# Performance work log

Measured on AMD Instinct MI355X. Metric: run time of the kernel, lower is better.

## Reference

```python
import jax, jax.numpy as jnp
import numpy as np

BS, NMEM, NQ, D, H, NL = 16, 256, 63, 512, 512, 1
INI = 0.01

def setup_inputs() -> dict:
    key = jax.random.key(0)
    ks = jax.random.split(key, 13)
    s_ih = 1.0 / np.sqrt(H)
    return {
        "knowledge_state": jax.random.normal(ks[0], (BS, NMEM, D), jnp.float32),
        "knowledge_num": jax.random.randint(ks[1], (BS,), 1, NMEM),
        "lstm_in": jax.random.normal(ks[2], (BS, NQ, D), jnp.float32),
        "init_h": jax.random.uniform(ks[3], (NL, H), jnp.float32, -INI, INI),
        "init_c": jax.random.uniform(ks[4], (NL, H), jnp.float32, -INI, INI),
        "init_i": jax.random.uniform(ks[5], (D,), jnp.float32, -0.1, 0.1),
        "w_ih": jax.random.uniform(ks[6], (4 * H, D), jnp.float32, -s_ih, s_ih),
        "w_hh": jax.random.uniform(ks[7], (4 * H, H), jnp.float32, -s_ih, s_ih),
        "b_ih": jax.random.uniform(ks[8], (4 * H,), jnp.float32, -s_ih, s_ih),
        "b_hh": jax.random.uniform(ks[9], (4 * H,), jnp.float32, -s_ih, s_ih),
        "attn_wm": jax.random.normal(ks[10], (D, H), jnp.float32) * np.sqrt(2.0 / (D + H)),
        "attn_wq": jax.random.normal(ks[11], (H, H), jnp.float32) * np.sqrt(2.0 / (H + H)),
        "attn_v": jax.random.uniform(ks[12], (H,), jnp.float32, -INI, INI),
    }


def _lstm(x_tbd, h0, c0, w_ih, w_hh, b_ih, b_hh):
    # x_tbd: [T, bs, D]; single-layer LSTM, PyTorch gate order (i, f, g, o)
    b = b_ih + b_hh

    def step(carry, x_t):
        h, c = carry
        gates = x_t @ w_ih.T + h @ w_hh.T + b  # [bs, 4H]
        i, f, g, o = jnp.split(gates, 4, axis=-1)
        c = jax.nn.sigmoid(f) * c + jax.nn.sigmoid(i) * jnp.tanh(g)
        h = jax.nn.sigmoid(o) * jnp.tanh(c)
        return (h, c), h

    _, ys = jax.lax.scan(step, (h0, c0), x_tbd)
    return ys  # [T, bs, H]


def reference(knowledge_state, knowledge_num, lstm_in, init_h, init_c, init_i,
              w_ih, w_hh, b_ih, b_hh, attn_wm, attn_wq, attn_v):
    bs = knowledge_state.shape[0]
    # _prepare: project memory, broadcast init states
    attn_feat = jnp.einsum('bmd,dh->bmh', knowledge_state, attn_wm)  # [bs, n_mem, H]
    # prepend learned init input token, go seq-first for the LSTM
    x = jnp.concatenate(
        [jnp.broadcast_to(init_i[None, None, :], (bs, 1, init_i.shape[0])), lstm_in],
        axis=1)                                   # [bs, T, D], T = n_q + 1
    x = jnp.swapaxes(x, 0, 1)                     # [T, bs, D]
    h0 = jnp.broadcast_to(init_h[0][None, :], (bs, init_h.shape[1]))
    c0 = jnp.broadcast_to(init_c[0][None, :], (bs, init_c.shape[1]))
    ys = _lstm(x, h0, c0, w_ih, w_hh, b_ih, b_hh)  # [T, bs, H]
    query = jnp.swapaxes(ys, 0, 1)                 # [bs, T, H]
    # additive (Bahdanau) attention score
    q = jnp.einsum('bth,hk->btk', query, attn_wq)  # [bs, T, H]
    s = jnp.tanh(attn_feat[:, None, :, :] + q[:, :, None, :])  # [bs, T, n_mem, H]
    score = jnp.einsum('btmh,h->btm', s, attn_v)   # [bs, T, n_mem]
    return score
```

## Files before the change

### kernel.cpp

```cpp
#include <hip/hip_runtime.h>

#define BS   16
#define NMEM 256
#define NQ   63
#define T    64
#define D    512
#define H    512
#define G4   2048

#define K2C  2.885390081777927f

typedef __attribute__((ext_vector_type(8))) short short8;
typedef __attribute__((ext_vector_type(4))) float float4v;

enum : size_t {
    OFF_XW  = 0,
    OFF_YS  = OFF_XW  + (size_t)T*BS*G4,
    OFF_HB  = OFF_YS  + (size_t)(T+1)*BS*H,
    OFF_AF  = OFF_HB  + (size_t)(T+1)*BS*H,
    OFF_Q   = OFF_AF  + (size_t)BS*NMEM*H,
    OFF_X   = OFF_Q   + (size_t)T*BS*H,
    OFF_B   = OFF_X   + (size_t)T*BS*D,
    OFF_BAR = OFF_B   + (size_t)G4,
};

__device__ inline unsigned short bf16_rn(float x) {
    union { float f; unsigned u; } a; a.f = x;
    unsigned r = a.u + 0x7FFFu + ((a.u >> 16) & 1u);
    return (unsigned short)(r >> 16);
}
__device__ inline float bf16_to_f(unsigned short s) {
    union { float f; unsigned u; } a; a.u = ((unsigned)s) << 16;
    return a.f;
}

__global__ void prep(const float* __restrict__ lstm_in, const float* __restrict__ init_h,
                     const float* __restrict__ init_i,
                     const float* __restrict__ b_ih, const float* __restrict__ b_hh,
                     float* __restrict__ xbuf, float* __restrict__ biasbuf,
                     unsigned short* __restrict__ hb0)
{
    int i = blockIdx.x * blockDim.x + threadIdx.x;
    const int NX = T*BS*D;
    if (i < NX) {
        int d = i & 511; int r = i >> 9; int t = r >> 4; int b = r & 15;
        float v = (t == 0) ? init_i[d] : lstm_in[((size_t)(b*NQ) + (t-1))*D + d];
        __builtin_nontemporal_store(v, xbuf + i);
    } else if (i < NX + G4) {
        int j = i - NX; biasbuf[j] = b_ih[j] + b_hh[j];
    } else if (i < NX + G4 + 8192) {
        int e = i - (NX + G4);
        int iw = e & 7;
        int k = ((e >> 3) >> 4) * 8 + iw;
        float h0 = init_h[k];
        unsigned short hi = bf16_rn(h0);
        unsigned short lo = bf16_rn(h0 - bf16_to_f(hi));
        hb0[e] = hi;
        hb0[8192 + e] = lo;
    }
}

template<bool BT>
__device__ inline void gemm_unit(const float* __restrict__ A, const float* __restrict__ B,
                                 float* __restrict__ C, const float* __restrict__ bias,
                                 int N, int K, int tm, int tn, int t2)
{
    const int w = t2 >> 6, lane = t2 & 63;
    const int quad = lane >> 4, l15 = lane & 15;
    const int am = tm + w*16 + l15;
    float4v acch[4] = {{0,0,0,0},{0,0,0,0},{0,0,0,0},{0,0,0,0}};
    float4v accl[4] = {{0,0,0,0},{0,0,0,0},{0,0,0,0},{0,0,0,0}};
    for (int k0 = 0; k0 < K; k0 += 32) {
        const float* ap = A + (size_t)am*K + k0 + quad*8;
        float4 a0 = *(const float4*)ap, a1 = *(const float4*)(ap+4);
        float av[8] = {a0.x,a0.y,a0.z,a0.w,a1.x,a1.y,a1.z,a1.w};
        short8 ah, al;
#pragma unroll
        for (int i = 0; i < 8; ++i) {
            unsigned short hi = bf16_rn(av[i]);
            ah[i] = (short)hi; al[i] = (short)bf16_rn(av[i] - bf16_to_f(hi));
        }
#pragma unroll
        for (int ni = 0; ni < 4; ++ni) {
            const int n = tn + ni*16 + l15;
            float bv[8];
            if (BT) {
                const float* bp = B + (size_t)n*K + k0 + quad*8;
                float4 b0 = *(const float4*)bp, b1 = *(const float4*)(bp+4);
                bv[0]=b0.x; bv[1]=b0.y; bv[2]=b0.z; bv[3]=b0.w;
                bv[4]=b1.x; bv[5]=b1.y; bv[6]=b1.z; bv[7]=b1.w;
            } else {
                const float* bp = B + (size_t)(k0 + quad*8)*N + n;
#pragma unroll
                for (int i = 0; i < 8; ++i) bv[i] = bp[(size_t)i*N];
            }
            short8 bh, bl;
#pragma unroll
            for (int i = 0; i < 8; ++i) {
                unsigned short hi = bf16_rn(bv[i]);
                bh[i] = (short)hi; bl[i] = (short)bf16_rn(bv[i] - bf16_to_f(hi));
            }
            acch[ni] = __builtin_amdgcn_mfma_f32_16x16x32_bf16(ah, bh, acch[ni], 0, 0, 0);
            accl[ni] = __builtin_amdgcn_mfma_f32_16x16x32_bf16(al, bh, accl[ni], 0, 0, 0);
            accl[ni] = __builtin_amdgcn_mfma_f32_16x16x32_bf16(ah, bl, accl[ni], 0, 0, 0);
        }
    }
#pragma unroll
    for (int ni = 0; ni < 4; ++ni) {
        const int n = tn + ni*16 + l15;
        float bb = bias ? bias[n] : 0.f;
        float4v r = acch[ni] + accl[ni];
#pragma unroll
        for (int j = 0; j < 4; ++j) {
            int row = tm + w*16 + quad*4 + j;
            __builtin_nontemporal_store(r[j] + bb, C + (size_t)row*N + n);
        }
    }
}

template<bool BT>
__global__ __launch_bounds__(256) void gemm_mfma(const float* __restrict__ A,
                                                 const float* __restrict__ B,
                                                 float* __restrict__ C,
                                                 const float* __restrict__ bias,
                                                 int N, int K)
{
    gemm_unit<BT>(A, B, C, bias, N, K, blockIdx.y*64, blockIdx.x*64, threadIdx.x);
}

__global__ __launch_bounds__(512, 2) void lstm_af(
    const float* __restrict__ xW,
    const float* __restrict__ w_hh,
    const float* __restrict__ init_c,
    const float* __restrict__ ks,
    const float* __restrict__ wm,
    float* __restrict__ ys,
    unsigned short* __restrict__ hbuf,
    float* __restrict__ af,
    int* __restrict__ flags)
{
    const int tid = threadIdx.x;

    if (blockIdx.x >= 32) {
        const int u = tid >> 8;
        const int tau = (blockIdx.x - 32)*2 + u;
        gemm_unit<false>(ks, wm, af, nullptr, H, D, (tau >> 3)*64, (tau & 7)*64, tid & 255);
        return;
    }

    __shared__ float smem[3328];
    float* part = smem;
    float* cst  = smem + 2048;
    float* xwb  = smem + 2304;

    const int jt    = blockIdx.x;
    const int w     = tid >> 6;
    const int g     = w >> 1;
    const int khalf = w & 1;
    const int lane  = tid & 63;
    const int quad  = lane >> 4;
    const int l15   = lane & 15;

    short8 bh[8], bl[8];
    {
        const int row = g*512 + jt*16 + l15;
        const float* wr = w_hh + (size_t)row*H + khalf*256 + quad*8;
#pragma unroll
        for (int kt = 0; kt < 8; ++kt) {
            const float* wp = wr + kt*32;
#pragma unroll
            for (int i = 0; i < 8; ++i) {
                float v = wp[i];
                unsigned short hi = bf16_rn(v);
                bh[kt][i] = (short)hi;
                bl[kt][i] = (short)bf16_rn(v - bf16_to_f(hi));
            }
        }
    }

    const int b2 = tid >> 4, j16 = tid & 15;
    if (tid < 256) cst[b2*16 + j16] = init_c[jt*16 + j16];
    if (tid >= 256) {
        int ti = tid - 256;
        int bb = ti >> 4, s = ti & 15;
        int gg = s & 3, j4 = (s >> 2) << 2;
        float4 v = *(const float4*)(xW + (size_t)bb*G4 + gg*512 + jt*16 + j4);
        float* dst = xwb + gg*256 + bb*16 + j4;
        dst[0]=v.x; dst[1]=v.y; dst[2]=v.z; dst[3]=v.w;
    }
    __syncthreads();

    for (int t = 0; t < T; ++t) {
        const unsigned short* hbt = hbuf + (size_t)t*16384;
        short8 ah[8], al[8];
#pragma unroll
        for (int kt = 0; kt < 8; ++kt) {
            int c = ((khalf*8 + kt)*4 + quad)*16 + l15;
            const unsigned short* p0 = hbt + (size_t)c*8;
            const unsigned short* p1 = p0 + 8192;
            asm volatile("global_load_dwordx4 %0, %1, off sc0 sc1"
                         : "=v"(ah[kt]) : "v"(p0) : "memory");
            asm volatile("global_load_dwordx4 %0, %1, off sc0 sc1"
                         : "=v"(al[kt]) : "v"(p1) : "memory");
        }
        asm volatile("s_waitcnt vmcnt(0)" ::: "memory");
        __builtin_amdgcn_sched_barrier(0);

        float4v a0 = {0.f,0.f,0.f,0.f}, a1 = {0.f,0.f,0.f,0.f};
#pragma unroll
        for (int kt = 0; kt < 8; ++kt) {
            a0 = __builtin_amdgcn_mfma_f32_16x16x32_bf16(ah[kt], bh[kt], a0, 0, 0, 0);
            a1 = __builtin_amdgcn_mfma_f32_16x16x32_bf16(al[kt], bh[kt], a1, 0, 0, 0);
            a1 = __builtin_amdgcn_mfma_f32_16x16x32_bf16(ah[kt], bl[kt], a1, 0, 0, 0);
        }
        a0 += a1;
        *(float4v*)&part[(w*64 + lane)*4] = a0;
        __syncthreads();

        if (tid < 256) {
            const int lsrc = ((b2 >> 2)*16 + j16)*4, r = b2 & 3;
            float gi = part[(0*256) + lsrc + r] + part[(1*256) + lsrc + r] + xwb[0*256 + b2*16 + j16];
            float gf = part[(2*256) + lsrc + r] + part[(3*256) + lsrc + r] + xwb[1*256 + b2*16 + j16];
            float gg = part[(4*256) + lsrc + r] + part[(5*256) + lsrc + r] + xwb[2*256 + b2*16 + j16];
            float go = part[(6*256) + lsrc + r] + part[(7*256) + lsrc + r] + xwb[3*256 + b2*16 + j16];
            float si = 1.f/(1.f+__expf(-gi));
            float sf = 1.f/(1.f+__expf(-gf));
            float so = 1.f/(1.f+__expf(-go));
            float cn = sf*cst[b2*16 + j16] + si*tanhf(gg);
            float hn = so*tanhf(cn);
            cst[b2*16 + j16] = cn;
            __builtin_nontemporal_store(hn, ys + (size_t)(t+1)*BS*H + b2*H + jt*16 + j16);
            const int k = jt*16 + j16;
            const int e = ((k >> 3)*16 + b2)*8 + (k & 7);
            unsigned short hi = bf16_rn(hn);
            unsigned int hv = (unsigned int)hi;
            unsigned int lv = (unsigned int)bf16_rn(hn - bf16_to_f(hi));
            unsigned short* hb1 = hbuf + (size_t)(t+1)*16384;
            asm volatile("global_store_short %0, %1, off sc0 sc1"
                         :: "v"(hb1 + e), "v"(hv) : "memory");
            asm volatile("global_store_short %0, %1, off sc0 sc1"
                         :: "v"(hb1 + 8192 + e), "v"(lv) : "memory");
            asm volatile("s_waitcnt vmcnt(0)" ::: "memory");
        }
        __syncthreads();

        if (t < T-1) {
            if (tid == 0) {
                int fv = t + 1;
                asm volatile("global_store_dword %0, %1, off sc0 sc1"
                             :: "v"(flags + jt*16), "v"(fv) : "memory");
            }
            if (tid >= 256) {
                int ti = tid - 256;
                int bb = ti >> 4, s = ti & 15;
                int gg2 = s & 3, j4 = (s >> 2) << 2;
                float4 v = *(const float4*)(xW + (size_t)(t+1)*BS*G4 + bb*G4 + gg2*512 + jt*16 + j4);
                float* dst = xwb + gg2*256 + bb*16 + j4;
                dst[0]=v.x; dst[1]=v.y; dst[2]=v.z; dst[3]=v.w;
            }
            if (tid < 64) {
                const int fidx = (tid & 31) << 4;
                const int* fp = flags + fidx;
                int v;
                do {
                    asm volatile("global_load_dword %0, %1, off sc0 sc1\n\t"
                                 "s_waitcnt vmcnt(0)"
                                 : "=v"(v) : "v"(fp) : "memory");
                } while (!__all(v >= t+1));
            }
            __syncthreads();
        }
    }
}

__global__ __launch_bounds__(256) void attn(const float* __restrict__ af,
                                            const float* __restrict__ q,
                                            const float* __restrict__ v,
                                            float* __restrict__ out)
{
    __shared__ float afs[64][68];
    __shared__ float qs[4][516];
    __shared__ float vs[512];
    const int tid = threadIdx.x;
    const int mc = blockIdx.x, tc = blockIdx.y, b = blockIdx.z;
    for (int i = tid; i < 4*128; i += 256) {
        int t = i >> 7, h4 = (i & 127) << 2;
        float4 x = *(const float4*)(q + ((size_t)((tc*4 + t)*16 + b) << 9) + h4);
        x.x *= K2C; x.y *= K2C; x.z *= K2C; x.w *= K2C;
        *(float4*)&qs[t][h4] = x;
    }
    for (int i = tid; i < 128; i += 256)
        *(float4*)&vs[i << 2] = *(const float4*)(v + (i << 2));
    const int ml = tid & 63, tg = tid >> 6;
    float acc = 0.f;
    for (int hc = 0; hc < 8; ++hc) {
        __syncthreads();
        for (int i = tid; i < 64*16; i += 256) {
            int m = i >> 4, h4 = (i & 15) << 2;
            float4 x = *(const float4*)(af + ((size_t)(b*NMEM + mc*64 + m) << 9) + hc*64 + h4);
            x.x *= K2C; x.y *= K2C; x.z *= K2C; x.w *= K2C;
            *(float4*)&afs[m][h4] = x;
        }
        __syncthreads();
#pragma unroll
        for (int h8 = 0; h8 < 8; ++h8) {
            float4 a0 = *(const float4*)&afs[ml][h8*8 + 0];
            float4 a1 = *(const float4*)&afs[ml][h8*8 + 4];
            float4 v0 = *(const float4*)&vs[hc*64 + h8*8 + 0];
            float4 v1 = *(const float4*)&vs[hc*64 + h8*8 + 4];
            float4 q0 = *(const float4*)&qs[tg][hc*64 + h8*8 + 0];
            float4 q1 = *(const float4*)&qs[tg][hc*64 + h8*8 + 4];
            const float* ap0 = (const float*)&a0; const float* ap1 = (const float*)&a1;
            const float* vp0 = (const float*)&v0; const float* vp1 = (const float*)&v1;
            const float* qp0 = (const float*)&q0; const float* qp1 = (const float*)&q1;
            float s = acc;
#pragma unroll
            for (int j = 0; j < 4; ++j) {
                float e = exp2f(ap0[j] + qp0[j]);
                s = fmaf(vp0[j], __builtin_amdgcn_rcpf(e + 1.f), s);
            }
#pragma unroll
            for (int j = 0; j < 4; ++j) {
                float e = exp2f(ap1[j] + qp1[j]);
                s = fmaf(vp1[j], __builtin_amdgcn_rcpf(e + 1.f), s);
            }
            acc = s;
        }
    }
    float Sv = 0.f;
    for (int i = 0; i < 512; i += 4) {
        float4 t4 = *(const float4*)&vs[i];
        Sv += t4.x + t4.y + t4.z + t4.w;
    }
    out[((size_t)b*T + tc*4 + tg)*NMEM + mc*64 + ml] = Sv - 2.f*acc;
}

extern "C" void kernel_launch(void* const* d_in, const int* in_sizes, int n_in,
                              void* d_out, int out_size, void* d_ws, size_t ws_size,
                              hipStream_t stream)
{
    const float* ks      = (const float*)d_in[0];
    const float* lstm_in = (const float*)d_in[2];
    const float* init_h  = (const float*)d_in[3];
    const float* init_c  = (const float*)d_in[4];
    const float* init_i  = (const float*)d_in[5];
    const float* w_ih    = (const float*)d_in[6];
    const float* w_hh    = (const float*)d_in[7];
    const float* b_ih    = (const float*)d_in[8];
    const float* b_hh    = (const float*)d_in[9];
    const float* wm      = (const float*)d_in[10];
    const float* wq      = (const float*)d_in[11];
    const float* av      = (const float*)d_in[12];

    float* ws   = (float*)d_ws;
    float* xW   = ws + OFF_XW;
    float* ys   = ws + OFF_YS;
    unsigned short* hbuf = (unsigned short*)(ws + OFF_HB);
    float* af   = ws + OFF_AF;
    float* qb   = ws + OFF_Q;
    float* xb   = ws + OFF_X;
    float* bias = ws + OFF_B;
    int*   flags= (int*)(ws + OFF_BAR);

    hipMemsetAsync(flags, 0, 512*sizeof(int), stream);

    const int prep_n = T*BS*D + G4 + 8192;
    prep<<<(prep_n + 255)/256, 256, 0, stream>>>(lstm_in, init_h, init_i,
                                                 b_ih, b_hh, xb, bias, hbuf);
    gemm_mfma<true><<<dim3(32, 16), 256, 0, stream>>>(xb, w_ih, xW, bias, G4, D);
    lstm_af<<<288, 512, 0, stream>>>(xW, w_hh, init_c, ks, wm, ys, hbuf, af, flags);
    gemm_mfma<false><<<dim3(8, 16), 256, 0, stream>>>(ys + BS*H, wq, qb, nullptr, H, H);
    attn<<<dim3(4, 16, 16), 256, 0, stream>>>(af, qb, av, (float*)d_out);
}
```

Measured before the change: 424.2 us.

## Replace flag barrier with sentinel-valued h buffer polling in persistent LSTM

Removes the per-step global flag store and spin-wait barrier. prep now fills every future hidden-state slot with a 0x7FFF sentinel, and each block re-loads its h fragments until no sentinel remains, so data arrival itself acts as the synchronization. Gate partials and the xW staging buffer are double-buffered in shared memory, the cell state is kept in a register, and the store wait plus one __syncthreads per step are dropped. Each step now costs extra sentinel checks and possible repeated loads, and correctness relies on no real bf16 hi or lo value equalling 0x7FFF (which is a NaN pattern).

```diff
diff --git a/kernel.cpp b/kernel.cpp
--- a/kernel.cpp
+++ b/kernel.cpp
@@ -12,6 +12,7 @@
 
 typedef __attribute__((ext_vector_type(8))) short short8;
 typedef __attribute__((ext_vector_type(4))) float float4v;
+typedef __attribute__((ext_vector_type(4))) unsigned int uint4v;
 
 enum : size_t {
     OFF_XW  = 0,
@@ -21,7 +22,6 @@
     OFF_Q   = OFF_AF  + (size_t)BS*NMEM*H,
     OFF_X   = OFF_Q   + (size_t)T*BS*H,
     OFF_B   = OFF_X   + (size_t)T*BS*D,
-    OFF_BAR = OFF_B   + (size_t)G4,
 };
 
 __device__ inline unsigned short bf16_rn(float x) {
@@ -42,13 +42,14 @@
 {
     int i = blockIdx.x * blockDim.x + threadIdx.x;
     const int NX = T*BS*D;
+    const int CAN0 = NX + G4 + 8192;
     if (i < NX) {
         int d = i & 511; int r = i >> 9; int t = r >> 4; int b = r & 15;
         float v = (t == 0) ? init_i[d] : lstm_in[((size_t)(b*NQ) + (t-1))*D + d];
         __builtin_nontemporal_store(v, xbuf + i);
     } else if (i < NX + G4) {
         int j = i - NX; biasbuf[j] = b_ih[j] + b_hh[j];
-    } else if (i < NX + G4 + 8192) {
+    } else if (i < CAN0) {
         int e = i - (NX + G4);
         int iw = e & 7;
         int k = ((e >> 3) >> 4) * 8 + iw;
@@ -57,6 +58,8 @@
         unsigned short lo = bf16_rn(h0 - bf16_to_f(hi));
         hb0[e] = hi;
         hb0[8192 + e] = lo;
+    } else if (i < CAN0 + T*8192) {
+        ((unsigned*)hb0)[8192 + (i - CAN0)] = 0x7FFF7FFFu;
     }
 }
 
@@ -136,8 +139,7 @@
     const float* __restrict__ wm,
     float* __restrict__ ys,
     unsigned short* __restrict__ hbuf,
-    float* __restrict__ af,
-    int* __restrict__ flags)
+    float* __restrict__ af)
 {
     const int tid = threadIdx.x;
 
@@ -148,10 +150,9 @@
         return;
     }
 
-    __shared__ float smem[3328];
+    __shared__ float smem[6144];
     float* part = smem;
-    float* cst  = smem + 2048;
-    float* xwb  = smem + 2304;
+    float* xwb  = smem + 4096;
 
     const int jt    = blockIdx.x;
     const int w     = tid >> 6;
@@ -179,7 +180,8 @@
     }
 
     const int b2 = tid >> 4, j16 = tid & 15;
-    if (tid < 256) cst[b2*16 + j16] = init_c[jt*16 + j16];
+    float creg = 0.f;
+    if (tid < 256) creg = init_c[jt*16 + j16];
     if (tid >= 256) {
         int ti = tid - 256;
         int bb = ti >> 4, s = ti & 15;
@@ -193,17 +195,33 @@
     for (int t = 0; t < T; ++t) {
         const unsigned short* hbt = hbuf + (size_t)t*16384;
         short8 ah[8], al[8];
-#pragma unroll
-        for (int kt = 0; kt < 8; ++kt) {
-            int c = ((khalf*8 + kt)*4 + quad)*16 + l15;
-            const unsigned short* p0 = hbt + (size_t)c*8;
-            const unsigned short* p1 = p0 + 8192;
-            asm volatile("global_load_dwordx4 %0, %1, off sc0 sc1"
-                         : "=v"(ah[kt]) : "v"(p0) : "memory");
-            asm volatile("global_load_dwordx4 %0, %1, off sc0 sc1"
-                         : "=v"(al[kt]) : "v"(p1) : "memory");
-        }
-        asm volatile("s_waitcnt vmcnt(0)" ::: "memory");
+        bool ok;
+        do {
+#pragma unroll
+            for (int kt = 0; kt < 8; ++kt) {
+                int c = ((khalf*8 + kt)*4 + quad)*16 + l15;
+                const unsigned short* p0 = hbt + (size_t)c*8;
+                const unsigned short* p1 = p0 + 8192;
+                asm volatile("global_load_dwordx4 %0, %1, off sc0 sc1"
+                             : "=v"(ah[kt]) : "v"(p0) : "memory");
+                asm volatile("global_load_dwordx4 %0, %1, off sc0 sc1"
+                             : "=v"(al[kt]) : "v"(p1) : "memory");
+            }
+            asm volatile("s_waitcnt vmcnt(0)" ::: "memory");
+            __builtin_amdgcn_sched_barrier(0);
+            ok = true;
+#pragma unroll
+            for (int kt = 0; kt < 8; ++kt) {
+                uint4v u0, u1;
+                __builtin_memcpy(&u0, &ah[kt], 16);
+                __builtin_memcpy(&u1, &al[kt], 16);
+#pragma unroll
+                for (int d2 = 0; d2 < 4; ++d2) {
+                    ok = ok && ((u0[d2] & 0xFFFFu) != 0x7FFFu) && ((u0[d2] >> 16) != 0x7FFFu);
+                    ok = ok && ((u1[d2] & 0xFFFFu) != 0x7FFFu) && ((u1[d2] >> 16) != 0x7FFFu);
+                }
+            }
+        } while (!ok);
         __builtin_amdgcn_sched_barrier(0);
 
         float4v a0 = {0.f,0.f,0.f,0.f}, a1 = {0.f,0.f,0.f,0.f};
@@ -214,21 +232,22 @@
             a1 = __builtin_amdgcn_mfma_f32_16x16x32_bf16(ah[kt], bl[kt], a1, 0, 0, 0);
         }
         a0 += a1;
-        *(float4v*)&part[(w*64 + lane)*4] = a0;
+        *(float4v*)&part[(t&1)*2048 + (w*64 + lane)*4] = a0;
         __syncthreads();
 
         if (tid < 256) {
+            const int pb = (t&1)*2048, xb0 = (t&1)*1024;
             const int lsrc = ((b2 >> 2)*16 + j16)*4, r = b2 & 3;
-            float gi = part[(0*256) + lsrc + r] + part[(1*256) + lsrc + r] + xwb[0*256 + b2*16 + j16];
-            float gf = part[(2*256) + lsrc + r] + part[(3*256) + lsrc + r] + xwb[1*256 + b2*16 + j16];
-            float gg = part[(4*256) + lsrc + r] + part[(5*256) + lsrc + r] + xwb[2*256 + b2*16 + j16];
-            float go = part[(6*256) + lsrc + r] + part[(7*256) + lsrc + r] + xwb[3*256 + b2*16 + j16];
+            float gi = part[pb + 0*256 + lsrc + r] + part[pb + 1*256 + lsrc + r] + xwb[xb0 + 0*256 + b2*16 + j16];
+            float gf = part[pb + 2*256 + lsrc + r] + part[pb + 3*256 + lsrc + r] + xwb[xb0 + 1*256 + b2*16 + j16];
+            float gg = part[pb + 4*256 + lsrc + r] + part[pb + 5*256 + lsrc + r] + xwb[xb0 + 2*256 + b2*16 + j16];
+            float go = part[pb + 6*256 + lsrc + r] + part[pb + 7*256 + lsrc + r] + xwb[xb0 + 3*256 + b2*16 + j16];
             float si = 1.f/(1.f+__expf(-gi));
             float sf = 1.f/(1.f+__expf(-gf));
             float so = 1.f/(1.f+__expf(-go));
-            float cn = sf*cst[b2*16 + j16] + si*tanhf(gg);
+            float cn = sf*creg + si*tanhf(gg);
             float hn = so*tanhf(cn);
-            cst[b2*16 + j16] = cn;
+            creg = cn;
             __builtin_nontemporal_store(hn, ys + (size_t)(t+1)*BS*H + b2*H + jt*16 + j16);
             const int k = jt*16 + j16;
             const int e = ((k >> 3)*16 + b2)*8 + (k & 7);
@@ -240,35 +259,14 @@
                          :: "v"(hb1 + e), "v"(hv) : "memory");
             asm volatile("global_store_short %0, %1, off sc0 sc1"
                          :: "v"(hb1 + 8192 + e), "v"(lv) : "memory");
-            asm volatile("s_waitcnt vmcnt(0)" ::: "memory");
-        }
-        __syncthreads();
-
-        if (t < T-1) {
-            if (tid == 0) {
-                int fv = t + 1;
-                asm volatile("global_store_dword %0, %1, off sc0 sc1"
-                             :: "v"(flags + jt*16), "v"(fv) : "memory");
-            }
-            if (tid >= 256) {
-                int ti = tid - 256;
-                int bb = ti >> 4, s = ti & 15;
-                int gg2 = s & 3, j4 = (s >> 2) << 2;
-                float4 v = *(const float4*)(xW + (size_t)(t+1)*BS*G4 + bb*G4 + gg2*512 + jt*16 + j4);
-                float* dst = xwb + gg2*256 + bb*16 + j4;
-                dst[0]=v.x; dst[1]=v.y; dst[2]=v.z; dst[3]=v.w;
-            }
-            if (tid < 64) {
-                const int fidx = (tid & 31) << 4;
-                const int* fp = flags + fidx;
-                int v;
-                do {
-                    asm volatile("global_load_dword %0, %1, off sc0 sc1\n\t"
-                                 "s_waitcnt vmcnt(0)"
-                                 : "=v"(v) : "v"(fp) : "memory");
-                } while (!__all(v >= t+1));
-            }
-            __syncthreads();
+        }
+        if (t < T-1 && tid >= 256) {
+            int ti = tid - 256;
+            int bb = ti >> 4, s = ti & 15;
+            int gg2 = s & 3, j4 = (s >> 2) << 2;
+            float4 v = *(const float4*)(xW + (size_t)(t+1)*BS*G4 + bb*G4 + gg2*512 + jt*16 + j4);
+            float* dst = xwb + ((t+1)&1)*1024 + gg2*256 + bb*16 + j4;
+            dst[0]=v.x; dst[1]=v.y; dst[2]=v.z; dst[3]=v.w;
         }
     }
 }
@@ -360,15 +358,12 @@
     float* qb   = ws + OFF_Q;
     float* xb   = ws + OFF_X;
     float* bias = ws + OFF_B;
-    int*   flags= (int*)(ws + OFF_BAR);
-
-    hipMemsetAsync(flags, 0, 512*sizeof(int), stream);
-
-    const int prep_n = T*BS*D + G4 + 8192;
+
+    const int prep_n = T*BS*D + G4 + 8192 + T*8192;
     prep<<<(prep_n + 255)/256, 256, 0, stream>>>(lstm_in, init_h, init_i,
                                                  b_ih, b_hh, xb, bias, hbuf);
     gemm_mfma<true><<<dim3(32, 16), 256, 0, stream>>>(xb, w_ih, xW, bias, G4, D);
-    lstm_af<<<288, 512, 0, stream>>>(xW, w_hh, init_c, ks, wm, ys, hbuf, af, flags);
+    lstm_af<<<288, 512, 0, stream>>>(xW, w_hh, init_c, ks, wm, ys, hbuf, af);
     gemm_mfma<false><<<dim3(8, 16), 256, 0, stream>>>(ys + BS*H, wq, qb, nullptr, H, H);
     attn<<<dim3(4, 16, 16), 256, 0, stream>>>(af, qb, av, (float*)d_out);
 }
```

Measured after the change: 799.4 us. 1.88x slower.

## Fuse query projection and attention into persistent LSTM kernel, overlapping with recurrence

Applied to the files above, without the earlier changes.

The 256 worker blocks that compute the memory projection now also compute the query projection and the attention scores inside the LSTM kernel. Each block handles one batch and a group of four timesteps, and it waits on the per-step flags until those LSTM steps have finished. This removes two kernel launches and lets the attention work overlap with the serial recurrence. The cost is a larger shared-memory footprint, bounded spin-waits with timeouts that could give wrong results if a timeout fires, a scalar FP32 q-projection in place of the MFMA GEMM, and ys stores that now bypass the cache.

```diff
diff --git a/kernel.cpp b/kernel.cpp
--- a/kernel.cpp
+++ b/kernel.cpp
@@ -9,6 +9,9 @@
 #define G4   2048
 
 #define K2C  2.885390081777927f
+
+#define SPIN_STEP (1u<<20)
+#define SPIN_JOIN (1u<<22)
 
 typedef __attribute__((ext_vector_type(8))) short short8;
 typedef __attribute__((ext_vector_type(4))) float float4v;
@@ -134,21 +137,141 @@
     const float* __restrict__ init_c,
     const float* __restrict__ ks,
     const float* __restrict__ wm,
+    const float* __restrict__ wq,
+    const float* __restrict__ av,
     float* __restrict__ ys,
     unsigned short* __restrict__ hbuf,
     float* __restrict__ af,
+    float* __restrict__ out,
     int* __restrict__ flags)
 {
     const int tid = threadIdx.x;
+    __shared__ float smem[13328];
 
     if (blockIdx.x >= 32) {
-        const int u = tid >> 8;
-        const int tau = (blockIdx.x - 32)*2 + u;
-        gemm_unit<false>(ks, wm, af, nullptr, H, D, (tau >> 3)*64, (tau & 7)*64, tid & 255);
+        const int wkr = blockIdx.x - 32;
+        const int u   = tid >> 8;
+        const int t2  = tid & 255;
+
+        const int tau = wkr*2 + u;
+        gemm_unit<false>(ks, wm, af, nullptr, H, D, (tau >> 3)*64, (tau & 7)*64, t2);
+
+        asm volatile("s_waitcnt vmcnt(0)" ::: "memory");
+        __syncthreads();
+        if (tid == 0) {
+            __hip_atomic_fetch_add(&flags[512], 1, __ATOMIC_RELEASE,
+                                   __HIP_MEMORY_SCOPE_AGENT);
+            int c; unsigned spin = 0;
+            do {
+                c = __hip_atomic_load(&flags[512], __ATOMIC_RELAXED,
+                                      __HIP_MEMORY_SCOPE_AGENT);
+            } while (c < 256 && ++spin < SPIN_JOIN);
+        }
+        __syncthreads();
+        __builtin_amdgcn_fence(__ATOMIC_ACQUIRE, "agent");
+
+        const int tc = wkr & 15, b = wkr >> 4;
+        const int tneed = tc*4 + 4;
+        if (tid < 64) {
+            const int fidx = (tid & 31) << 4;
+            const int* fp = flags + fidx;
+            int v; unsigned spin = 0;
+            do {
+                asm volatile("global_load_dword %0, %1, off sc0 sc1\n\t"
+                             "s_waitcnt vmcnt(0)"
+                             : "=v"(v) : "v"(fp) : "memory");
+            } while (!__all(v >= tneed) && ++spin < SPIN_STEP);
+        }
+        __syncthreads();
+
+        float* afs0 = smem;
+        float* afs1 = smem + 4352;
+        float* qs   = smem + 8704;
+        float* vs   = smem + 10768;
+        float* ysb  = smem + 11280;
+
+        {
+            float yv0, yv1, yv2, yv3;
+            const float* y0p = ys + (((size_t)(tc*4 + 1)*16) + b)*512 + tid;
+            const float* y1p = y0p + (size_t)16*512;
+            const float* y2p = y1p + (size_t)16*512;
+            const float* y3p = y2p + (size_t)16*512;
+            asm volatile("global_load_dword %0, %1, off sc0 sc1" : "=v"(yv0) : "v"(y0p) : "memory");
+            asm volatile("global_load_dword %0, %1, off sc0 sc1" : "=v"(yv1) : "v"(y1p) : "memory");
+            asm volatile("global_load_dword %0, %1, off sc0 sc1" : "=v"(yv2) : "v"(y2p) : "memory");
+            asm volatile("global_load_dword %0, %1, off sc0 sc1" : "=v"(yv3) : "v"(y3p) : "memory");
+            asm volatile("s_waitcnt vmcnt(0)" ::: "memory");
+            __builtin_amdgcn_sched_barrier(0);
+            ysb[0*512 + tid] = yv0; ysb[1*512 + tid] = yv1;
+            ysb[2*512 + tid] = yv2; ysb[3*512 + tid] = yv3;
+        }
+        vs[tid & 511] = av[tid & 511];
+        __syncthreads();
+
+        {
+            float q0=0.f, q1=0.f, q2=0.f, q3=0.f;
+            for (int k = 0; k < 512; ++k) {
+                float wv = wq[(size_t)k*512 + tid];
+                float y0 = ysb[k], y1 = ysb[512+k], y2 = ysb[1024+k], y3 = ysb[1536+k];
+                q0 = fmaf(y0, wv, q0); q1 = fmaf(y1, wv, q1);
+                q2 = fmaf(y2, wv, q2); q3 = fmaf(y3, wv, q3);
+            }
+            qs[0*516 + tid] = q0*K2C; qs[1*516 + tid] = q1*K2C;
+            qs[2*516 + tid] = q2*K2C; qs[3*516 + tid] = q3*K2C;
+        }
+        __syncthreads();
+
+        float Sv = 0.f;
+        for (int i = 0; i < 512; i += 4) {
+            float4 t4 = *(const float4*)&vs[i];
+            Sv += t4.x + t4.y + t4.z + t4.w;
+        }
+
+        float* afs_u = u ? afs1 : afs0;
+        const int ml = t2 & 63, tg = t2 >> 6;
+#pragma unroll
+        for (int mcidx = 0; mcidx < 2; ++mcidx) {
+            const int mc = u + mcidx*2;
+            float acc = 0.f;
+            for (int hc = 0; hc < 8; ++hc) {
+                __syncthreads();
+                for (int i = t2; i < 64*16; i += 256) {
+                    int m = i >> 4, h4 = (i & 15) << 2;
+                    float4 x = *(const float4*)(af + ((size_t)(b*NMEM + mc*64 + m) << 9) + hc*64 + h4);
+                    x.x *= K2C; x.y *= K2C; x.z *= K2C; x.w *= K2C;
+                    *(float4*)&afs_u[m*68 + h4] = x;
+                }
+                __syncthreads();
+#pragma unroll
+                for (int h8 = 0; h8 < 8; ++h8) {
+                    float4 a0 = *(const float4*)&afs_u[ml*68 + h8*8 + 0];
+                    float4 a1 = *(const float4*)&afs_u[ml*68 + h8*8 + 4];
+                    float4 v0 = *(const float4*)&vs[hc*64 + h8*8 + 0];
+                    float4 v1 = *(const float4*)&vs[hc*64 + h8*8 + 4];
+                    float4 q0 = *(const float4*)&qs[tg*516 + hc*64 + h8*8 + 0];
+                    float4 q1 = *(const float4*)&qs[tg*516 + hc*64 + h8*8 + 4];
+                    const float* ap0 = (const float*)&a0; const float* ap1 = (const float*)&a1;
+                    const float* vp0 = (const float*)&v0; const float* vp1 = (const float*)&v1;
+                    const float* qp0 = (const float*)&q0; const float* qp1 = (const float*)&q1;
+                    float s = acc;
+#pragma unroll
+                    for (int j = 0; j < 4; ++j) {
+                        float e = exp2f(ap0[j] + qp0[j]);
+                        s = fmaf(vp0[j], __builtin_amdgcn_rcpf(e + 1.f), s);
+                    }
+#pragma unroll
+                    for (int j = 0; j < 4; ++j) {
+                        float e = exp2f(ap1[j] + qp1[j]);
+                        s = fmaf(vp1[j], __builtin_amdgcn_rcpf(e + 1.f), s);
+                    }
+                    acc = s;
+                }
+            }
+            out[((size_t)b*T + tc*4 + tg)*NMEM + mc*64 + ml] = Sv - 2.f*acc;
+        }
         return;
     }
 
-    __shared__ float smem[3328];
     float* part = smem;
     float* cst  = smem + 2048;
     float* xwb  = smem + 2304;
@@ -229,7 +352,9 @@
             float cn = sf*cst[b2*16 + j16] + si*tanhf(gg);
             float hn = so*tanhf(cn);
             cst[b2*16 + j16] = cn;
-            __builtin_nontemporal_store(hn, ys + (size_t)(t+1)*BS*H + b2*H + jt*16 + j16);
+            const float* ysp = ys + (size_t)(t+1)*BS*H + b2*H + jt*16 + j16;
+            asm volatile("global_store_dword %0, %1, off sc0 sc1"
+                         :: "v"(ysp), "v"(hn) : "memory");
             const int k = jt*16 + j16;
             const int e = ((k >> 3)*16 + b2)*8 + (k & 7);
             unsigned short hi = bf16_rn(hn);
@@ -244,12 +369,12 @@
         }
         __syncthreads();
 
+        if (tid == 0) {
+            int fv = t + 1;
+            asm volatile("global_store_dword %0, %1, off sc0 sc1"
+                         :: "v"(flags + jt*16), "v"(fv) : "memory");
+        }
         if (t < T-1) {
-            if (tid == 0) {
-                int fv = t + 1;
-                asm volatile("global_store_dword %0, %1, off sc0 sc1"
-                             :: "v"(flags + jt*16), "v"(fv) : "memory");
-            }
             if (tid >= 256) {
                 int ti = tid - 256;
                 int bb = ti >> 4, s = ti & 15;
@@ -261,78 +386,16 @@
             if (tid < 64) {
                 const int fidx = (tid & 31) << 4;
                 const int* fp = flags + fidx;
-                int v;
+                int v; unsigned spin = 0;
                 do {
                     asm volatile("global_load_dword %0, %1, off sc0 sc1\n\t"
                                  "s_waitcnt vmcnt(0)"
                                  : "=v"(v) : "v"(fp) : "memory");
-                } while (!__all(v >= t+1));
+                } while (!__all(v >= t+1) && ++spin < SPIN_STEP);
             }
             __syncthreads();
         }
     }
-}
-
-__global__ __launch_bounds__(256) void attn(const float* __restrict__ af,
-                                            const float* __restrict__ q,
-                                            const float* __restrict__ v,
-                                            float* __restrict__ out)
-{
-    __shared__ float afs[64][68];
-    __shared__ float qs[4][516];
-    __shared__ float vs[512];
-    const int tid = threadIdx.x;
-    const int mc = blockIdx.x, tc = blockIdx.y, b = blockIdx.z;
-    for (int i = tid; i < 4*128; i += 256) {
-        int t = i >> 7, h4 = (i & 127) << 2;
-        float4 x = *(const float4*)(q + ((size_t)((tc*4 + t)*16 + b) << 9) + h4);
-        x.x *= K2C; x.y *= K2C; x.z *= K2C; x.w *= K2C;
-        *(float4*)&qs[t][h4] = x;
-    }
-    for (int i = tid; i < 128; i += 256)
-        *(float4*)&vs[i << 2] = *(const float4*)(v + (i << 2));
-    const int ml = tid & 63, tg = tid >> 6;
-    float acc = 0.f;
-    for (int hc = 0; hc < 8; ++hc) {
-        __syncthreads();
-        for (int i = tid; i < 64*16; i += 256) {
-            int m = i >> 4, h4 = (i & 15) << 2;
-            float4 x = *(const float4*)(af + ((size_t)(b*NMEM + mc*64 + m) << 9) + hc*64 + h4);
-            x.x *= K2C; x.y *= K2C; x.z *= K2C; x.w *= K2C;
-            *(float4*)&afs[m][h4] = x;
-        }
-        __syncthreads();
-#pragma unroll
-        for (int h8 = 0; h8 < 8; ++h8) {
-            float4 a0 = *(const float4*)&afs[ml][h8*8 + 0];
-            float4 a1 = *(const float4*)&afs[ml][h8*8 + 4];
-            float4 v0 = *(const float4*)&vs[hc*64 + h8*8 + 0];
-            float4 v1 = *(const float4*)&vs[hc*64 + h8*8 + 4];
-            float4 q0 = *(const float4*)&qs[tg][hc*64 + h8*8 + 0];
-            float4 q1 = *(const float4*)&qs[tg][hc*64 + h8*8 + 4];
-            const float* ap0 = (const float*)&a0; const float* ap1 = (const float*)&a1;
-            const float* vp0 = (const float*)&v0; const float* vp1 = (const float*)&v1;
-            const float* qp0 = (const float*)&q0; const float* qp1 = (const float*)&q1;
-            float s = acc;
-#pragma unroll
-            for (int j = 0; j < 4; ++j) {
-                float e = exp2f(ap0[j] + qp0[j]);
-                s = fmaf(vp0[j], __builtin_amdgcn_rcpf(e + 1.f), s);
-            }
-#pragma unroll
-            for (int j = 0; j < 4; ++j) {
-                float e = exp2f(ap1[j] + qp1[j]);
-                s = fmaf(vp1[j], __builtin_amdgcn_rcpf(e + 1.f), s);
-            }
-            acc = s;
-        }
-    }
-    float Sv = 0.f;
-    for (int i = 0; i < 512; i += 4) {
-        float4 t4 = *(const float4*)&vs[i];
-        Sv += t4.x + t4.y + t4.z + t4.w;
-    }
-    out[((size_t)b*T + tc*4 + tg)*NMEM + mc*64 + ml] = Sv - 2.f*acc;
 }
 
 extern "C" void kernel_launch(void* const* d_in, const int* in_sizes, int n_in,
@@ -357,18 +420,16 @@
     float* ys   = ws + OFF_YS;
     unsigned short* hbuf = (unsigned short*)(ws + OFF_HB);
     float* af   = ws + OFF_AF;
-    float* qb   = ws + OFF_Q;
     float* xb   = ws + OFF_X;
     float* bias = ws + OFF_B;
     int*   flags= (int*)(ws + OFF_BAR);
 
-    hipMemsetAsync(flags, 0, 512*sizeof(int), stream);
+    hipMemsetAsync(flags, 0, 768*sizeof(int), stream);
 
     const int prep_n = T*BS*D + G4 + 8192;
     prep<<<(prep_n + 255)/256, 256, 0, stream>>>(lstm_in, init_h, init_i,
                                                  b_ih, b_hh, xb, bias, hbuf);
     gemm_mfma<true><<<dim3(32, 16), 256, 0, stream>>>(xb, w_ih, xW, bias, G4, D);
-    lstm_af<<<288, 512, 0, stream>>>(xW, w_hh, init_c, ks, wm, ys, hbuf, af, flags);
-    gemm_mfma<false><<<dim3(8, 16), 256, 0, stream>>>(ys + BS*H, wq, qb, nullptr, H, H);
-    attn<<<dim3(4, 16, 16), 256, 0, stream>>>(af, qb, av, (float*)d_out);
-}
+    lstm_af<<<288, 512, 0, stream>>>(xW, w_hh, init_c, ks, wm, wq, av,
+                                     ys, hbuf, af, (float*)d_out, flags);
+}
```

Measured after the change: 501.6 us. 1.18x slower.
